# Kernel tuning notes

Hardware: AMD Instinct MI355X
Metric: run time of the kernel (lower is better)

## Reference

```python
import jax, jax.numpy as jnp
import numpy as np

MARGIN = 0.3
BIG = 1e30  # finite sentinel for masked max/min (avoids inf-inf NaNs)


def setup_inputs() -> dict:
    key = jax.random.key(0)
    k1, k2 = jax.random.split(key)
    N, D = 8192, 128
    embeddings = jax.random.normal(k1, (N, D), dtype=jnp.float32)
    labels = jax.random.randint(k2, (N,), 0, 1024, dtype=jnp.int64)
    return {"embeddings": embeddings, "labels": labels}


def _pairwise_euclidean(x):
    # torch.cdist(x, x, p=2): sqrt of clamped squared distances,
    # with a double-where so sqrt(0) has no NaN gradient.
    sq = jnp.sum(x * x, axis=1)                      # [N]
    d2 = sq[:, None] + sq[None, :] - 2.0 * (x @ x.T)  # [N, N]
    d2 = jnp.maximum(d2, 0.0)
    safe = jnp.where(d2 > 0.0, d2, 1.0)
    return jnp.where(d2 > 0.0, jnp.sqrt(safe), 0.0)


def reference(embeddings, labels):
    dist = _pairwise_euclidean(embeddings)           # [N, N]
    same = labels[:, None] == labels[None, :]        # [N, N]
    eye = jnp.eye(labels.shape[0], dtype=bool)
    mask_pos = same & ~eye
    mask_neg = ~same

    hardest_pos = jnp.max(jnp.where(mask_pos, dist, -BIG), axis=1)  # [N]
    hardest_neg = jnp.min(jnp.where(mask_neg, dist, BIG), axis=1)   # [N]

    valid = jnp.any(mask_pos, axis=1) & jnp.any(mask_neg, axis=1)
    per_row = jax.nn.relu(hardest_pos - hardest_neg + MARGIN)
    per_row = jnp.where(valid, per_row, 0.0)
    cnt = jnp.sum(valid.astype(jnp.float32))
    # torch code returns 0.0 when no valid anchors
    return jnp.where(cnt > 0, jnp.sum(per_row) / jnp.maximum(cnt, 1.0), 0.0)
```

## Files before the change

kernel.cpp:

```cpp
#include <hip/hip_runtime.h>
#include <hip/hip_bf16.h>

#define NSPLIT 16
#define BIGF 1e30f
#define MARGIN 0.3f
#define DK 128

typedef __attribute__((ext_vector_type(8))) short bf16x8;
typedef __attribute__((ext_vector_type(4))) float f32x4;

#define WS_HIST 0
#define WS_GSUM 1024
#define WS_GCNT 1025
#define WS_BCNT 1026
#define WS_HP   1028
#define WS_HN   (WS_HP + 8192)
#define WS_SQ   (WS_HN + 8192)
#define WS_XB   (WS_SQ + 8192)
#define WS_ZERO_BYTES (1028 * 4)


__global__ __launch_bounds__(256) void prep_kernel(
    const float* __restrict__ x, ushort* __restrict__ xs,
    float* __restrict__ sq, unsigned* __restrict__ hist,
    const int* __restrict__ lab,
    unsigned* __restrict__ hp_bits, unsigned* __restrict__ hn_comp, int N)
{
    const int tid = threadIdx.x;
    const int rbase = blockIdx.x * 32;
    const int rl = tid >> 4;
    const int kc = tid & 15;

    #pragma unroll
    for (int g = 0; g < 2; ++g) {
        int row = rbase + g * 16 + rl;
        const float4* p = (const float4*)(x + (size_t)row * DK + kc * 8);
        float4 u = p[0], v = p[1];
        float f[8] = {u.x, u.y, u.z, u.w, v.x, v.y, v.z, v.w};
        union { bf16x8 v8; ushort us[8]; } o;
        float ps = 0.0f;
        #pragma unroll
        for (int e = 0; e < 8; ++e) {
            __hip_bfloat16 b = __float2bfloat16(f[e]);
            o.us[e] = *(ushort*)&b;
            ps += f[e] * f[e];
        }
        ((bf16x8*)xs)[(size_t)(row >> 4) * 256 + kc * 16 + rl] = o.v8;
        #pragma unroll
        for (int o2 = 8; o2 > 0; o2 >>= 1) ps += __shfl_xor(ps, o2, 16);
        if (kc == 0) {
            sq[row] = ps;
            hp_bits[row] = 0u;
            hn_comp[row] = 0u;
            atomicAdd(&hist[lab[row]], 1u);
        }
    }
}


#define LOADB(B, SQB, LB, CH)                                             \
    {                                                                     \
        const unsigned cb = (unsigned)cbegin + (unsigned)(CH) * 16;       \
        const ushort* bp = xs + (size_t)cb * DK + quad * 128 + m16 * 8;   \
        _Pragma("unroll")                                                 \
        for (int s = 0; s < 4; ++s)                                       \
            B[s] = *(const bf16x8*)(bp + s * 512);                        \
        int colg = (int)cb + m16;                                         \
        SQB = sq[colg]; LB = lab[colg];                                   \
    }

#define MFMA_CHUNK(B)                                                     \
    _Pragma("unroll")                                                     \
    for (int s = 0; s < 4; ++s)                                           \
        _Pragma("unroll")                                                 \
        for (int mt = 0; mt < 2; ++mt)                                    \
            acc[mt] = __builtin_amdgcn_mfma_f32_16x16x32_bf16(            \
                afr[mt][s], B[s],                                         \
                (s == 0) ? (f32x4){0.f, 0.f, 0.f, 0.f} : acc[mt],         \
                0, 0, 0);

#define EPI_CHUNK(SQB, LB)                                                \
    _Pragma("unroll")                                                     \
    for (int mt = 0; mt < 2; ++mt)                                        \
        _Pragma("unroll")                                                 \
        for (int r = 0; r < 4; ++r) {                                     \
            float t = fmaf(-2.0f, acc[mt][r], SQB);                       \
            bool sm = (rlv[mt][r] == LB);                                 \
            runhp[mt][r] = fmaxf(runhp[mt][r], sm ? t : -BIGF);           \
            runhn[mt][r] = fminf(runhn[mt][r], sm ? BIGF : t);            \
        }

__global__ __launch_bounds__(256, 4) void tile_kernel(
    const ushort* __restrict__ xs, const float* __restrict__ sq,
    const int* __restrict__ lab,
    unsigned* __restrict__ hp_bits, unsigned* __restrict__ hn_comp, int N)
{
    const int tid  = threadIdx.x;
    const int lane = tid & 63;
    const int wave = tid >> 6;
    const int m16  = lane & 15;
    const int quad = lane >> 4;
    const int rbase  = blockIdx.x * 128 + wave * 32;
    const int cbegin = blockIdx.y * (N / NSPLIT);

    bf16x8 afr[2][4];
    {
        const ushort* ap = xs + (size_t)rbase * DK + quad * 128 + m16 * 8;
        #pragma unroll
        for (int mt = 0; mt < 2; ++mt)
            #pragma unroll
            for (int s = 0; s < 4; ++s)
                afr[mt][s] = *(const bf16x8*)(ap + mt * 2048 + s * 512);
    }

    int rlv[2][4];
    #pragma unroll
    for (int mt = 0; mt < 2; ++mt) {
        int4 v = *(const int4*)(lab + rbase + mt * 16 + quad * 4);
        rlv[mt][0] = v.x; rlv[mt][1] = v.y; rlv[mt][2] = v.z; rlv[mt][3] = v.w;
    }

    float runhp[2][4], runhn[2][4];
    #pragma unroll
    for (int mt = 0; mt < 2; ++mt)
        #pragma unroll
        for (int r = 0; r < 4; ++r) { runhp[mt][r] = -BIGF; runhn[mt][r] = BIGF; }

    bf16x8 bX[4], bY[4];
    float sqX, sqY;
    int lbX, lbY;
    f32x4 acc[2];

    LOADB(bX, sqX, lbX, 0);

    #pragma unroll 1
    for (int k = 0; k < 32; k += 2) {
        LOADB(bY, sqY, lbY, k + 1);
        MFMA_CHUNK(bX);
        EPI_CHUNK(sqX, lbX);
        LOADB(bX, sqX, lbX, (k + 2 < 32) ? k + 2 : 31);
        MFMA_CHUNK(bY);
        EPI_CHUNK(sqY, lbY);
    }

    #pragma unroll
    for (int mt = 0; mt < 2; ++mt)
        #pragma unroll
        for (int r = 0; r < 4; ++r) {
            #pragma unroll
            for (int o = 8; o > 0; o >>= 1) {
                runhp[mt][r] = fmaxf(runhp[mt][r], __shfl_xor(runhp[mt][r], o, 16));
                runhn[mt][r] = fminf(runhn[mt][r], __shfl_xor(runhn[mt][r], o, 16));
            }
        }

    if (m16 == 0) {
        #pragma unroll
        for (int mt = 0; mt < 2; ++mt)
            #pragma unroll
            for (int r = 0; r < 4; ++r) {
                int row = rbase + mt * 16 + quad * 4 + r;
                float sqa = sq[row];
                float d2p = fmaxf(sqa + runhp[mt][r], 0.0f);
                float d2n = fmaxf(sqa + runhn[mt][r], 0.0f);
                atomicMax(&hp_bits[row], __float_as_uint(d2p));
                atomicMax(&hn_comp[row], ~__float_as_uint(d2n));
            }
    }
}

__global__ void finalize_kernel(const unsigned* __restrict__ hp_bits,
                                const unsigned* __restrict__ hn_comp,
                                const int* __restrict__ lab,
                                const unsigned* __restrict__ hist,
                                float* __restrict__ gsum, float* __restrict__ gcnt,
                                unsigned* __restrict__ bcount,
                                float* __restrict__ out, int N)
{
    __shared__ float s_sum[256];
    __shared__ float s_cnt[256];
    int tid = threadIdx.x;
    int row = blockIdx.x * 256 + tid;
    float loss = 0.0f, cv = 0.0f;
    if (row < N) {
        unsigned c = hist[lab[row]];
        bool valid = (c >= 2u) && (c < (unsigned)N);
        if (valid) {
            float dp = sqrtf(__uint_as_float(hp_bits[row]));
            float dn = sqrtf(__uint_as_float(~hn_comp[row]));
            loss = fmaxf(dp - dn + MARGIN, 0.0f);
            cv = 1.0f;
        }
    }
    s_sum[tid] = loss; s_cnt[tid] = cv;
    __syncthreads();
    for (int o = 128; o > 0; o >>= 1) {
        if (tid < o) { s_sum[tid] += s_sum[tid + o]; s_cnt[tid] += s_cnt[tid + o]; }
        __syncthreads();
    }
    if (tid == 0) {
        atomicAdd(gsum, s_sum[0]);
        atomicAdd(gcnt, s_cnt[0]);
        __threadfence();
        unsigned old = atomicAdd(bcount, 1u);
        if (old == gridDim.x - 1) {
            float s = atomicAdd(gsum, 0.0f);
            float c = atomicAdd(gcnt, 0.0f);
            out[0] = (c > 0.0f) ? s / c : 0.0f;
        }
    }
}

extern "C" void kernel_launch(void* const* d_in, const int* in_sizes, int n_in,
                              void* d_out, int out_size, void* d_ws, size_t ws_size,
                              hipStream_t stream) {
    const float* x = (const float*)d_in[0];
    const int* lab = (const int*)d_in[1];
    float* out = (float*)d_out;
    const int N = in_sizes[1];

    unsigned* ws = (unsigned*)d_ws;
    unsigned* hist    = ws + WS_HIST;
    float* gsum = (float*)(ws + WS_GSUM);
    float* gcnt = (float*)(ws + WS_GCNT);
    unsigned* bcount = ws + WS_BCNT;
    unsigned* hp_bits = ws + WS_HP;
    unsigned* hn_comp = ws + WS_HN;
    float* sq = (float*)(ws + WS_SQ);
    ushort* xs = (ushort*)(ws + WS_XB);

    hipMemsetAsync(d_ws, 0, (size_t)WS_ZERO_BYTES, stream);
    prep_kernel<<<N / 32, 256, 0, stream>>>(x, xs, sq, hist, lab, hp_bits, hn_comp, N);
    dim3 grid(N / 128, NSPLIT);
    tile_kernel<<<grid, 256, 0, stream>>>(xs, sq, lab, hp_bits, hn_comp, N);
    finalize_kernel<<<N / 256, 256, 0, stream>>>(hp_bits, hn_comp, lab, hist,
                                                 gsum, gcnt, bcount, out, N);
}
```

Measured before the change: 95.99 us.

## Exploit distance-matrix symmetry by computing only upper-triangle tiles with column reductions

Switches the tile kernel from a row-block by column-split grid to 128x128 tiles covering only about half of the block pairs, using a cyclic diagonal mapping. Each tile now reduces both per-row and per-column hardest positive/negative values, with the column results combined across waves in shared memory and sent through atomics. This roughly halves the MFMA work of the symmetric Gram matrix. In exchange it adds per-element epilogue work, cross-lane shuffles and twice as many atomics. It also lowers the occupancy hint from 4 to 2 blocks per SM and launches many more, smaller blocks. With NB/2+1 offsets and NB even, the offset-NB/2 tiles are computed twice, which is redundant but harmless for max/min.

```diff
diff --git a/kernel.cpp b/kernel.cpp
--- a/kernel.cpp
+++ b/kernel.cpp
@@ -1,7 +1,6 @@
 #include <hip/hip_runtime.h>
 #include <hip/hip_bf16.h>
 
-#define NSPLIT 16
 #define BIGF 1e30f
 #define MARGIN 0.3f
 #define DK 128
@@ -60,7 +59,7 @@
 
 #define LOADB(B, SQB, LB, CH)                                             \
     {                                                                     \
-        const unsigned cb = (unsigned)cbegin + (unsigned)(CH) * 16;       \
+        const unsigned cb = (unsigned)cbase + (unsigned)(CH) * 16;        \
         const ushort* bp = xs + (size_t)cb * DK + quad * 128 + m16 * 8;   \
         _Pragma("unroll")                                                 \
         for (int s = 0; s < 4; ++s)                                       \
@@ -79,29 +78,50 @@
                 (s == 0) ? (f32x4){0.f, 0.f, 0.f, 0.f} : acc[mt],         \
                 0, 0, 0);
 
-#define EPI_CHUNK(SQB, LB)                                                \
-    _Pragma("unroll")                                                     \
-    for (int mt = 0; mt < 2; ++mt)                                        \
+#define EPI_CHUNK(CH, SQB, LB)                                            \
+    {                                                                     \
+        float cph = -BIGF, cnh = BIGF;                                    \
         _Pragma("unroll")                                                 \
-        for (int r = 0; r < 4; ++r) {                                     \
-            float t = fmaf(-2.0f, acc[mt][r], SQB);                       \
-            bool sm = (rlv[mt][r] == LB);                                 \
-            runhp[mt][r] = fmaxf(runhp[mt][r], sm ? t : -BIGF);           \
-            runhn[mt][r] = fminf(runhn[mt][r], sm ? BIGF : t);            \
-        }
-
-__global__ __launch_bounds__(256, 4) void tile_kernel(
+        for (int mt = 0; mt < 2; ++mt)                                    \
+            _Pragma("unroll")                                             \
+            for (int r = 0; r < 4; ++r) {                                 \
+                float d = acc[mt][r];                                     \
+                float t  = fmaf(-2.0f, d, SQB);                           \
+                float tc = fmaf(-2.0f, d, sqa[mt][r]);                    \
+                bool sm = (rlv[mt][r] == LB);                             \
+                runhp[mt][r] = fmaxf(runhp[mt][r], sm ? t : -BIGF);       \
+                runhn[mt][r] = fminf(runhn[mt][r], sm ? BIGF : t);        \
+                cph = fmaxf(cph, sm ? tc : -BIGF);                        \
+                cnh = fminf(cnh, sm ? BIGF : tc);                         \
+            }                                                             \
+        cph = fmaxf(cph, __shfl_xor(cph, 16, 64));                        \
+        cph = fmaxf(cph, __shfl_xor(cph, 32, 64));                        \
+        cnh = fminf(cnh, __shfl_xor(cnh, 16, 64));                        \
+        cnh = fminf(cnh, __shfl_xor(cnh, 32, 64));                        \
+        if (lane < 16) {                                                  \
+            colhp_s[wave][(CH) * 16 + m16] = cph;                         \
+            colhn_s[wave][(CH) * 16 + m16] = cnh;                         \
+        }                                                                 \
+    }
+
+__global__ __launch_bounds__(256, 2) void tile_kernel(
     const ushort* __restrict__ xs, const float* __restrict__ sq,
     const int* __restrict__ lab,
     unsigned* __restrict__ hp_bits, unsigned* __restrict__ hn_comp, int N)
 {
+    __shared__ float colhp_s[4][128];
+    __shared__ float colhn_s[4][128];
+
     const int tid  = threadIdx.x;
     const int lane = tid & 63;
     const int wave = tid >> 6;
     const int m16  = lane & 15;
     const int quad = lane >> 4;
-    const int rbase  = blockIdx.x * 128 + wave * 32;
-    const int cbegin = blockIdx.y * (N / NSPLIT);
+    const int NB   = N >> 7;
+    const int bi   = blockIdx.x;
+    const int bj   = (int)((blockIdx.x + blockIdx.y) % (unsigned)NB);
+    const int rbase = bi * 128 + wave * 32;
+    const int cbase = bj * 128;
 
     bf16x8 afr[2][4];
     {
@@ -113,11 +133,13 @@
                 afr[mt][s] = *(const bf16x8*)(ap + mt * 2048 + s * 512);
     }
 
-    int rlv[2][4];
+    int rlv[2][4]; float sqa[2][4];
     #pragma unroll
     for (int mt = 0; mt < 2; ++mt) {
         int4 v = *(const int4*)(lab + rbase + mt * 16 + quad * 4);
         rlv[mt][0] = v.x; rlv[mt][1] = v.y; rlv[mt][2] = v.z; rlv[mt][3] = v.w;
+        float4 s4 = *(const float4*)(sq + rbase + mt * 16 + quad * 4);
+        sqa[mt][0] = s4.x; sqa[mt][1] = s4.y; sqa[mt][2] = s4.z; sqa[mt][3] = s4.w;
     }
 
     float runhp[2][4], runhn[2][4];
@@ -134,13 +156,13 @@
     LOADB(bX, sqX, lbX, 0);
 
     #pragma unroll 1
-    for (int k = 0; k < 32; k += 2) {
+    for (int k = 0; k < 8; k += 2) {
         LOADB(bY, sqY, lbY, k + 1);
         MFMA_CHUNK(bX);
-        EPI_CHUNK(sqX, lbX);
-        LOADB(bX, sqX, lbX, (k + 2 < 32) ? k + 2 : 31);
+        EPI_CHUNK(k, sqX, lbX);
+        LOADB(bX, sqX, lbX, (k + 2 < 8) ? k + 2 : 7);
         MFMA_CHUNK(bY);
-        EPI_CHUNK(sqY, lbY);
+        EPI_CHUNK(k + 1, sqY, lbY);
     }
 
     #pragma unroll
@@ -160,12 +182,25 @@
             #pragma unroll
             for (int r = 0; r < 4; ++r) {
                 int row = rbase + mt * 16 + quad * 4 + r;
-                float sqa = sq[row];
-                float d2p = fmaxf(sqa + runhp[mt][r], 0.0f);
-                float d2n = fmaxf(sqa + runhn[mt][r], 0.0f);
+                float d2p = fmaxf(sqa[mt][r] + runhp[mt][r], 0.0f);
+                float d2n = fmaxf(sqa[mt][r] + runhn[mt][r], 0.0f);
                 atomicMax(&hp_bits[row], __float_as_uint(d2p));
                 atomicMax(&hn_comp[row], ~__float_as_uint(d2n));
             }
+    }
+
+    __syncthreads();
+    if (tid < 128) {
+        float thp = fmaxf(fmaxf(colhp_s[0][tid], colhp_s[1][tid]),
+                          fmaxf(colhp_s[2][tid], colhp_s[3][tid]));
+        float thn = fminf(fminf(colhn_s[0][tid], colhn_s[1][tid]),
+                          fminf(colhn_s[2][tid], colhn_s[3][tid]));
+        int col = cbase + tid;
+        float sqc = sq[col];
+        float d2p = fmaxf(sqc + thp, 0.0f);
+        float d2n = fmaxf(sqc + thn, 0.0f);
+        atomicMax(&hp_bits[col], __float_as_uint(d2p));
+        atomicMax(&hn_comp[col], ~__float_as_uint(d2n));
     }
 }
 
@@ -231,7 +266,8 @@
 
     hipMemsetAsync(d_ws, 0, (size_t)WS_ZERO_BYTES, stream);
     prep_kernel<<<N / 32, 256, 0, stream>>>(x, xs, sq, hist, lab, hp_bits, hn_comp, N);
-    dim3 grid(N / 128, NSPLIT);
+    const int NB = N / 128;
+    dim3 grid(NB, NB / 2 + 1);
     tile_kernel<<<grid, 256, 0, stream>>>(xs, sq, lab, hp_bits, hn_comp, N);
     finalize_kernel<<<N / 256, 256, 0, stream>>>(hp_bits, hn_comp, lab, hist,
                                                  gsum, gcnt, bcount, out, N);
```

After: 95.23 us. About the same (-0.8%).

## Double row tile per wave, drop memset, move label histogram into tile kernel

Applied to the files above, without the earlier changes.

Each wave now computes 64 rows instead of 32, so every loaded B fragment feeds four MFMA row tiles. This halves B-operand global traffic per output and the tile grid shrinks to N/256 x 16 blocks with occupancy hint 2. The hipMemsetAsync is removed: prep_kernel zeroes the histogram and the scalar accumulators itself, and the label histogram atomics move into the tile kernel's blockIdx.y==0 blocks, which run after prep in stream order. Risks are higher register pressure, fewer resident waves, and the zeroing depending on the prep grid covering all 1024 histogram bins (N/32*4 = 1024).

```diff
diff --git a/kernel.cpp b/kernel.cpp
--- a/kernel.cpp
+++ b/kernel.cpp
@@ -17,19 +17,23 @@
 #define WS_HN   (WS_HP + 8192)
 #define WS_SQ   (WS_HN + 8192)
 #define WS_XB   (WS_SQ + 8192)
-#define WS_ZERO_BYTES (1028 * 4)
 
 
 __global__ __launch_bounds__(256) void prep_kernel(
     const float* __restrict__ x, ushort* __restrict__ xs,
     float* __restrict__ sq, unsigned* __restrict__ hist,
-    const int* __restrict__ lab,
+    unsigned* __restrict__ scal,
     unsigned* __restrict__ hp_bits, unsigned* __restrict__ hn_comp, int N)
 {
     const int tid = threadIdx.x;
     const int rbase = blockIdx.x * 32;
     const int rl = tid >> 4;
     const int kc = tid & 15;
+
+    if (tid < 4) {
+        hist[blockIdx.x * 4 + tid] = 0u;
+        if (blockIdx.x == 0) scal[tid] = 0u;
+    }
 
     #pragma unroll
     for (int g = 0; g < 2; ++g) {
@@ -52,7 +56,6 @@
             sq[row] = ps;
             hp_bits[row] = 0u;
             hn_comp[row] = 0u;
-            atomicAdd(&hist[lab[row]], 1u);
         }
     }
 }
@@ -73,7 +76,7 @@
     _Pragma("unroll")                                                     \
     for (int s = 0; s < 4; ++s)                                           \
         _Pragma("unroll")                                                 \
-        for (int mt = 0; mt < 2; ++mt)                                    \
+        for (int mt = 0; mt < 4; ++mt)                                    \
             acc[mt] = __builtin_amdgcn_mfma_f32_16x16x32_bf16(            \
                 afr[mt][s], B[s],                                         \
                 (s == 0) ? (f32x4){0.f, 0.f, 0.f, 0.f} : acc[mt],         \
@@ -81,7 +84,7 @@
 
 #define EPI_CHUNK(SQB, LB)                                                \
     _Pragma("unroll")                                                     \
-    for (int mt = 0; mt < 2; ++mt)                                        \
+    for (int mt = 0; mt < 4; ++mt)                                        \
         _Pragma("unroll")                                                 \
         for (int r = 0; r < 4; ++r) {                                     \
             float t = fmaf(-2.0f, acc[mt][r], SQB);                       \
@@ -90,9 +93,9 @@
             runhn[mt][r] = fminf(runhn[mt][r], sm ? BIGF : t);            \
         }
 
-__global__ __launch_bounds__(256, 4) void tile_kernel(
+__global__ __launch_bounds__(256, 2) void tile_kernel(
     const ushort* __restrict__ xs, const float* __restrict__ sq,
-    const int* __restrict__ lab,
+    const int* __restrict__ lab, unsigned* __restrict__ hist,
     unsigned* __restrict__ hp_bits, unsigned* __restrict__ hn_comp, int N)
 {
     const int tid  = threadIdx.x;
@@ -100,51 +103,54 @@
     const int wave = tid >> 6;
     const int m16  = lane & 15;
     const int quad = lane >> 4;
-    const int rbase  = blockIdx.x * 128 + wave * 32;
+    const int rbase  = blockIdx.x * 256 + wave * 64;
     const int cbegin = blockIdx.y * (N / NSPLIT);
 
-    bf16x8 afr[2][4];
+    bf16x8 afr[4][4];
     {
         const ushort* ap = xs + (size_t)rbase * DK + quad * 128 + m16 * 8;
         #pragma unroll
-        for (int mt = 0; mt < 2; ++mt)
+        for (int mt = 0; mt < 4; ++mt)
             #pragma unroll
             for (int s = 0; s < 4; ++s)
                 afr[mt][s] = *(const bf16x8*)(ap + mt * 2048 + s * 512);
     }
 
-    int rlv[2][4];
-    #pragma unroll
-    for (int mt = 0; mt < 2; ++mt) {
+    if (blockIdx.y == 0)
+        atomicAdd(&hist[lab[blockIdx.x * 256 + tid]], 1u);
+
+    int rlv[4][4];
+    #pragma unroll
+    for (int mt = 0; mt < 4; ++mt) {
         int4 v = *(const int4*)(lab + rbase + mt * 16 + quad * 4);
         rlv[mt][0] = v.x; rlv[mt][1] = v.y; rlv[mt][2] = v.z; rlv[mt][3] = v.w;
     }
 
-    float runhp[2][4], runhn[2][4];
-    #pragma unroll
-    for (int mt = 0; mt < 2; ++mt)
+    float runhp[4][4], runhn[4][4];
+    #pragma unroll
+    for (int mt = 0; mt < 4; ++mt)
         #pragma unroll
         for (int r = 0; r < 4; ++r) { runhp[mt][r] = -BIGF; runhn[mt][r] = BIGF; }
 
-    bf16x8 bX[4], bY[4];
-    float sqX, sqY;
-    int lbX, lbY;
-    f32x4 acc[2];
-
-    LOADB(bX, sqX, lbX, 0);
+    bf16x8 bA[4], bB[4];
+    float sqA, sqB;
+    int lbA, lbB;
+    f32x4 acc[4];
+
+    LOADB(bA, sqA, lbA, 0);
 
     #pragma unroll 1
     for (int k = 0; k < 32; k += 2) {
-        LOADB(bY, sqY, lbY, k + 1);
-        MFMA_CHUNK(bX);
-        EPI_CHUNK(sqX, lbX);
-        LOADB(bX, sqX, lbX, (k + 2 < 32) ? k + 2 : 31);
-        MFMA_CHUNK(bY);
-        EPI_CHUNK(sqY, lbY);
-    }
-
-    #pragma unroll
-    for (int mt = 0; mt < 2; ++mt)
+        LOADB(bB, sqB, lbB, k + 1);
+        MFMA_CHUNK(bA);
+        EPI_CHUNK(sqA, lbA);
+        LOADB(bA, sqA, lbA, (k + 2 < 32) ? k + 2 : 31);
+        MFMA_CHUNK(bB);
+        EPI_CHUNK(sqB, lbB);
+    }
+
+    #pragma unroll
+    for (int mt = 0; mt < 4; ++mt)
         #pragma unroll
         for (int r = 0; r < 4; ++r) {
             #pragma unroll
@@ -156,7 +162,7 @@
 
     if (m16 == 0) {
         #pragma unroll
-        for (int mt = 0; mt < 2; ++mt)
+        for (int mt = 0; mt < 4; ++mt)
             #pragma unroll
             for (int r = 0; r < 4; ++r) {
                 int row = rbase + mt * 16 + quad * 4 + r;
@@ -221,6 +227,7 @@
 
     unsigned* ws = (unsigned*)d_ws;
     unsigned* hist    = ws + WS_HIST;
+    unsigned* scal    = ws + WS_GSUM;
     float* gsum = (float*)(ws + WS_GSUM);
     float* gcnt = (float*)(ws + WS_GCNT);
     unsigned* bcount = ws + WS_BCNT;
@@ -229,10 +236,9 @@
     float* sq = (float*)(ws + WS_SQ);
     ushort* xs = (ushort*)(ws + WS_XB);
 
-    hipMemsetAsync(d_ws, 0, (size_t)WS_ZERO_BYTES, stream);
-    prep_kernel<<<N / 32, 256, 0, stream>>>(x, xs, sq, hist, lab, hp_bits, hn_comp, N);
-    dim3 grid(N / 128, NSPLIT);
-    tile_kernel<<<grid, 256, 0, stream>>>(xs, sq, lab, hp_bits, hn_comp, N);
+    prep_kernel<<<N / 32, 256, 0, stream>>>(x, xs, sq, hist, scal, hp_bits, hn_comp, N);
+    dim3 grid(N / 256, NSPLIT);
+    tile_kernel<<<grid, 256, 0, stream>>>(xs, sq, lab, hist, hp_bits, hn_comp, N);
     finalize_kernel<<<N / 256, 256, 0, stream>>>(hp_bits, hn_comp, lab, hist,
                                                  gsum, gcnt, bcount, out, N);
 }
```

New measurement: 104.5 us. 1.09x slower.
